# Performance work log

Hardware: AMD Instinct MI355X
Metric: run time of the kernel (lower is better)

## Reference

```python
import jax, jax.numpy as jnp
import numpy as np

N_NODES = 100000


def setup_inputs() -> dict:
    key = jax.random.key(0)
    ks = jax.random.split(key, 9)
    E = 1600000
    x = jax.random.normal(ks[0], (N_NODES, 12), dtype=jnp.float32)
    edge_index = jax.random.randint(ks[1], (2, E), 0, N_NODES, dtype=jnp.int64)
    def glorot(k, shape):
        lim = float(np.sqrt(6.0 / (shape[0] + shape[1])))
        return jax.random.uniform(k, shape, jnp.float32, -lim, lim)
    return {
        "x": x,
        "edge_index": edge_index,
        "W1": glorot(ks[2], (12, 64)),
        "b1": jnp.zeros((64,), jnp.float32),
        "W2": glorot(ks[3], (64, 128)),
        "b2": jnp.zeros((128,), jnp.float32),
        "W3": glorot(ks[4], (128, 96)),
        "b3": jnp.zeros((96,), jnp.float32),
    }


def reference(x, edge_index, W1, b1, W2, b2, W3, b3):
    N = x.shape[0]
    F_channel, n_his = 8, 12
    src, dst = edge_index[0], edge_index[1]
    # add self loops (PyG GCNConv default)
    loop = jnp.arange(N, dtype=src.dtype)
    src = jnp.concatenate([src, loop])
    dst = jnp.concatenate([dst, loop])
    # symmetric normalization: norm_e = deg[src]^-1/2 * deg[dst]^-1/2
    deg = jax.ops.segment_sum(jnp.ones_like(src, dtype=x.dtype), dst, num_segments=N)
    dinv = jnp.where(deg > 0, jax.lax.rsqrt(deg), 0.0)
    norm = dinv[src] * dinv[dst]  # [E+N]

    def gcn(h, W, b):
        hw = h @ W  # transform first (out_ch <= in-edge fanout cost)
        agg = jax.ops.segment_sum(hw[src] * norm[:, None], dst, num_segments=N)
        return agg + b

    h = jax.nn.relu(gcn(x, W1, b1))
    h = jax.nn.relu(gcn(h, W2, b2))
    h = gcn(h, W3, b3)
    return h.reshape(N, F_channel, n_his)
```

## Files before the change

### kernel.cpp

```cpp
#include <hip/hip_runtime.h>
#include <hip/hip_bf16.h>
#include <hip/hip_fp16.h>


static inline int cdiv(int a, int b) { return (a + b - 1) / b; }
constexpr int BLOCK = 256;
constexpr int BSHIFT = 9;
constexpr int BNODES = 1 << BSHIFT;

typedef float nfloat4 __attribute__((ext_vector_type(4)));
typedef _Float16 f16x8 __attribute__((ext_vector_type(8)));
typedef float f32x16 __attribute__((ext_vector_type(16)));


__global__ void zero_int_kernel(int* __restrict__ p, int n) {
    int i = blockIdx.x * blockDim.x + threadIdx.x;
    if (i < n) p[i] = 0;
}

__device__ __forceinline__ void nt_store_raw16(void* p, float4 v) {
    nfloat4 nv;
    nv.x = v.x; nv.y = v.y; nv.z = v.z; nv.w = v.w;
    __builtin_nontemporal_store(nv, (nfloat4*)p);
}

struct h4 { __half2 a, b; };
__device__ __forceinline__ void store_h4(__half* p, float4 v) {
    h4 r;
    r.a = __floats2half2_rn(v.x, v.y);
    r.b = __floats2half2_rn(v.z, v.w);
    *(h4*)p = r;
}

__device__ __forceinline__ void h8_add(float* acc, float4 raw) {
    union { float4 f; __half2 h[4]; } u;
    u.f = raw;
#pragma unroll
    for (int j = 0; j < 4; ++j) {
        float2 p = __half22float2(u.h[j]);
        acc[2 * j] += p.x;
        acc[2 * j + 1] += p.y;
    }
}


template <int CHUNK>
__global__ void bucket_count_kernel(const int* __restrict__ dst, int E,
                                    int* __restrict__ bcnt, int NB) {
    __shared__ int cnt[256];
    for (int i = threadIdx.x; i < NB; i += blockDim.x) cnt[i] = 0;
    __syncthreads();
    const int e0 = blockIdx.x * CHUNK;
    const int e1 = min(e0 + CHUNK, E);
    for (int e = e0 + threadIdx.x; e < e1; e += blockDim.x)
        atomicAdd(&cnt[dst[e] >> BSHIFT], 1);
    __syncthreads();
    for (int i = threadIdx.x; i < NB; i += blockDim.x)
        if (cnt[i]) atomicAdd(&bcnt[i], cnt[i]);
}

__global__ void bucket_scan_kernel(const int* __restrict__ bcnt, int* __restrict__ gbase,
                                   int* __restrict__ gcur, int NB) {
    __shared__ int tmp[256];
    int t = threadIdx.x;
    int v = (t < NB) ? bcnt[t] : 0;
    tmp[t] = v;
    __syncthreads();
    for (int off = 1; off < 256; off <<= 1) {
        int add = (t >= off) ? tmp[t - off] : 0;
        __syncthreads();
        tmp[t] += add;
        __syncthreads();
    }
    if (t < NB) { int ex = tmp[t] - v; gbase[t] = ex; gcur[t] = ex; }
}

template <int CHUNK>
__global__ void bin_edges_kernel(const int* __restrict__ ei, int E,
                                 int* __restrict__ gcur, unsigned* __restrict__ binned,
                                 int NB) {
    __shared__ int cnt[256], base[256], rk[256];
    for (int i = threadIdx.x; i < NB; i += blockDim.x) { cnt[i] = 0; rk[i] = 0; }
    __syncthreads();
    const int e0 = blockIdx.x * CHUNK;
    const int e1 = min(e0 + CHUNK, E);
    for (int e = e0 + threadIdx.x; e < e1; e += blockDim.x)
        atomicAdd(&cnt[ei[E + e] >> BSHIFT], 1);
    __syncthreads();
    for (int i = threadIdx.x; i < NB; i += blockDim.x)
        base[i] = atomicAdd(&gcur[i], cnt[i]);
    __syncthreads();
    for (int e = e0 + threadIdx.x; e < e1; e += blockDim.x) {
        int s = ei[e], d = ei[E + e];
        int b = d >> BSHIFT;
        int r = atomicAdd(&rk[b], 1);
        binned[base[b] + r] = (unsigned)s | ((unsigned)(d & (BNODES - 1)) << 17);
    }
}

__global__ void csr_fill_kernel(const int* __restrict__ gbase, const int* __restrict__ bcnt,
                                const unsigned* __restrict__ binned,
                                int* __restrict__ deg, float* __restrict__ dinv,
                                int* __restrict__ row_ptr, int* __restrict__ csr_src,
                                int* __restrict__ dh, int N) {
    __shared__ int c[BNODES];
    __shared__ int ps[256];
    __shared__ int dhloc[64];
    const int t = threadIdx.x;
    const int b = blockIdx.x;
    const int node0 = b << BSHIFT;
    c[t] = 0; c[t + 256] = 0;
    if (t < 64) dhloc[t] = 0;
    __syncthreads();
    const int base = gbase[b];
    const int end = base + bcnt[b];
    for (int e = base + t; e < end; e += 256)
        atomicAdd(&c[binned[e] >> 17], 1);
    __syncthreads();
    const int s0 = c[2 * t], s1 = c[2 * t + 1];
    const int pv = s0 + s1;
    ps[t] = pv;
    __syncthreads();
    for (int off = 1; off < 256; off <<= 1) {
        int add = (t >= off) ? ps[t - off] : 0;
        __syncthreads();
        ps[t] += add;
        __syncthreads();
    }
    const int ex = ps[t] - pv;
    const int p0 = base + ex;
    const int p1 = p0 + s0;
    const int n0 = node0 + 2 * t;
    if (n0 < N) {
        row_ptr[n0] = p0; deg[n0] = s0; dinv[n0] = rsqrtf((float)s0 + 1.0f);
        atomicAdd(&dhloc[min(s0, 63)], 1);
        if (n0 + 1 < N) {
            row_ptr[n0 + 1] = p1; deg[n0 + 1] = s1; dinv[n0 + 1] = rsqrtf((float)s1 + 1.0f);
            atomicAdd(&dhloc[min(s1, 63)], 1);
        }
    }
    c[2 * t] = p0; c[2 * t + 1] = p1;
    __syncthreads();
    if (t < 64 && dhloc[t]) atomicAdd(&dh[t], dhloc[t]);
    for (int e = base + t; e < end; e += 256) {
        unsigned sd = binned[e];
        int pos = atomicAdd(&c[sd >> 17], 1);
        csr_src[pos] = (int)(sd & 0x1FFFFu);
    }
}


__global__ void dscan_kernel(int* __restrict__ dh) {
    __shared__ int tmp[64];
    int t = threadIdx.x;
    int v = dh[t];
    tmp[t] = v;
    __syncthreads();
    for (int off = 1; off < 64; off <<= 1) {
        int add = (t >= off) ? tmp[t - off] : 0;
        __syncthreads();
        tmp[t] += add;
        __syncthreads();
    }
    dh[t] = tmp[t] - v;
}

__global__ void dperm_kernel(const int* __restrict__ deg, int* __restrict__ dh,
                             int* __restrict__ perm, int N) {
    __shared__ int cnt[64], base[64], rk[64];
    const int t = threadIdx.x;
    if (t < 64) { cnt[t] = 0; rk[t] = 0; }
    __syncthreads();
    const int i = blockIdx.x * blockDim.x + t;
    const int myb = (i < N) ? min(deg[i], 63) : -1;
    if (myb >= 0) atomicAdd(&cnt[myb], 1);
    __syncthreads();
    if (t < 64) base[t] = cnt[t] ? atomicAdd(&dh[t], cnt[t]) : 0;
    __syncthreads();
    if (myb >= 0) {
        int r = atomicAdd(&rk[myb], 1);
        perm[base[myb] + r] = i;
    }
}


__global__ void prescale_h_kernel(const float* __restrict__ x, const float* __restrict__ dinv,
                                  __half* __restrict__ xs, int N) {
    int i = blockIdx.x * blockDim.x + threadIdx.x;
    if (i >= N) return;
    float di = dinv[i];
    const float4* xr = (const float4*)(x + (size_t)i * 12);
    float4 a = xr[0], b = xr[1], c = xr[2];
    union { float4 f; __half2 h[4]; } u0, u1;
    u0.h[0] = __floats2half2_rn(a.x * di, a.y * di);
    u0.h[1] = __floats2half2_rn(a.z * di, a.w * di);
    u0.h[2] = __floats2half2_rn(b.x * di, b.y * di);
    u0.h[3] = __floats2half2_rn(b.z * di, b.w * di);
    u1.h[0] = __floats2half2_rn(c.x * di, c.y * di);
    u1.h[1] = __floats2half2_rn(c.z * di, c.w * di);
    u1.h[2] = __floats2half2_rn(0.f, 0.f);
    u1.h[3] = __floats2half2_rn(0.f, 0.f);
    float4* op = (float4*)(xs + (size_t)i * 16);
    op[0] = u0.f;
    op[1] = u1.f;
}


__device__ __forceinline__ void fma4(float4& acc, float s, const float4& w) {
    acc.x = fmaf(s, w.x, acc.x);
    acc.y = fmaf(s, w.y, acc.y);
    acc.z = fmaf(s, w.z, acc.z);
    acc.w = fmaf(s, w.w, acc.w);
}

__device__ __forceinline__ float4 epilogue4(float4 r, const float* bias, int c0,
                                            bool has_bias, bool relu, bool scale, float di) {
    if (has_bias) {
        const float4 bb = *(const float4*)(bias + c0);
        r.x += bb.x; r.y += bb.y; r.z += bb.z; r.w += bb.w;
    }
    if (relu) {
        r.x = fmaxf(r.x, 0.f); r.y = fmaxf(r.y, 0.f);
        r.z = fmaxf(r.z, 0.f); r.w = fmaxf(r.w, 0.f);
    }
    if (scale) { r.x *= di; r.y *= di; r.z *= di; r.w *= di; }
    return r;
}

template <int IN, int OUT, bool HAS_BIAS, bool RELU, bool SCALE, bool OUT_HALF>
__global__ void transform_kernel(const float* __restrict__ h, const float* __restrict__ W,
                                 const float* __restrict__ bias, const float* __restrict__ dinv,
                                 void* __restrict__ out_v, int N) {
    constexpr int CG = OUT / 4;
    constexpr int THREADS = 8 * CG;
    __shared__ float Ws[IN * OUT];
    for (int i = threadIdx.x; i < IN * OUT / 4; i += THREADS)
        ((float4*)Ws)[i] = ((const float4*)W)[i];
    __syncthreads();

    const int c0 = (threadIdx.x % CG) * 4;
    const int r0 = blockIdx.x * 32 + (threadIdx.x / CG) * 4;
    if (r0 >= N) return;

    const float* __restrict__ hr = h + (size_t)r0 * IN;
    float4 acc[4];
#pragma unroll
    for (int i = 0; i < 4; ++i) acc[i] = make_float4(0.f, 0.f, 0.f, 0.f);

#pragma unroll
    for (int k = 0; k < IN; k += 4) {
        float4 a[4];
#pragma unroll
        for (int i = 0; i < 4; ++i) a[i] = *(const float4*)(hr + (size_t)i * IN + k);
        const float4 w0 = *(const float4*)(Ws + (k + 0) * OUT + c0);
        const float4 w1 = *(const float4*)(Ws + (k + 1) * OUT + c0);
        const float4 w2 = *(const float4*)(Ws + (k + 2) * OUT + c0);
        const float4 w3 = *(const float4*)(Ws + (k + 3) * OUT + c0);
#pragma unroll
        for (int i = 0; i < 4; ++i) {
            fma4(acc[i], a[i].x, w0);
            fma4(acc[i], a[i].y, w1);
            fma4(acc[i], a[i].z, w2);
            fma4(acc[i], a[i].w, w3);
        }
    }

#pragma unroll
    for (int i = 0; i < 4; ++i) {
        float di = SCALE ? dinv[r0 + i] : 0.f;
        float4 r = epilogue4(acc[i], bias, c0, HAS_BIAS, RELU, SCALE, di);
        if (OUT_HALF)
            store_h4((__half*)out_v + (size_t)(r0 + i) * OUT + c0, r);
        else
            *(float4*)((float*)out_v + (size_t)(r0 + i) * OUT + c0) = r;
    }
}


__global__ void prep_w_kernel(const float* __restrict__ W2, const float* __restrict__ W3,
                              __half* __restrict__ W2T, __half* __restrict__ W3T) {
    int i = blockIdx.x * 256 + threadIdx.x;
    if (i < 64 * 128) {
        int k = i >> 7, n = i & 127;
        W2T[n * 64 + k] = __float2half(W2[i]);
    } else {
        int j = i - 64 * 128;
        if (j < 128 * 96) {
            int k = j / 96, n = j - k * 96;
            W3T[n * 128 + k] = __float2half(W3[j]);
        }
    }
}

__global__ void fused_t2t3_kernel(const __half* __restrict__ agg1,
                                  const __half* __restrict__ W2T,
                                  const float* __restrict__ b2,
                                  const __half* __restrict__ W3T,
                                  const float* __restrict__ dinv,
                                  __half* __restrict__ out,
                                  int N) {
    constexpr int LDH = 136;
    __shared__ _Float16 h2s[4][32 * LDH];
    const int lane = threadIdx.x & 63;
    const int wid = threadIdx.x >> 6;
    const int l31 = lane & 31;
    const int lh = lane >> 5;
    _Float16* hs = h2s[wid];

    float b2v[4];
#pragma unroll
    for (int nt = 0; nt < 4; ++nt) b2v[nt] = b2[nt * 32 + l31];

    const int NT = N >> 5;
    for (int t = blockIdx.x * 4 + wid; t < NT; t += gridDim.x * 4) {
        const int r0 = t << 5;

        f16x8 a2[4];
#pragma unroll
        for (int kb = 0; kb < 4; ++kb)
            a2[kb] = *(const f16x8*)(agg1 + (size_t)(r0 + l31) * 64 + kb * 16 + lh * 8);
#pragma unroll
        for (int nt = 0; nt < 4; ++nt) {
            f32x16 c = {0.f, 0.f, 0.f, 0.f, 0.f, 0.f, 0.f, 0.f,
                        0.f, 0.f, 0.f, 0.f, 0.f, 0.f, 0.f, 0.f};
#pragma unroll
            for (int kb = 0; kb < 4; ++kb) {
                f16x8 b = *(const f16x8*)(W2T + (size_t)(nt * 32 + l31) * 64 + kb * 16 + lh * 8);
                c = __builtin_amdgcn_mfma_f32_32x32x16_f16(a2[kb], b, c, 0, 0, 0);
            }
#pragma unroll
            for (int r = 0; r < 16; ++r) {
                int row = (r & 3) + 8 * (r >> 2) + 4 * lh;
                float v = fmaxf(c[r] + b2v[nt], 0.f);
                hs[row * LDH + nt * 32 + l31] = (_Float16)v;
            }
        }

        f16x8 a3[8];
#pragma unroll
        for (int kb = 0; kb < 8; ++kb)
            a3[kb] = *(const f16x8*)(hs + l31 * LDH + kb * 16 + lh * 8);
        float4 dv[4];
#pragma unroll
        for (int rg = 0; rg < 4; ++rg)
            dv[rg] = *(const float4*)(dinv + r0 + rg * 8 + lh * 4);
#pragma unroll
        for (int nt = 0; nt < 3; ++nt) {
            f32x16 c = {0.f, 0.f, 0.f, 0.f, 0.f, 0.f, 0.f, 0.f,
                        0.f, 0.f, 0.f, 0.f, 0.f, 0.f, 0.f, 0.f};
#pragma unroll
            for (int kb = 0; kb < 8; ++kb) {
                f16x8 b = *(const f16x8*)(W3T + (size_t)(nt * 32 + l31) * 128 + kb * 16 + lh * 8);
                c = __builtin_amdgcn_mfma_f32_32x32x16_f16(a3[kb], b, c, 0, 0, 0);
            }
#pragma unroll
            for (int r = 0; r < 16; ++r) {
                int row = (r & 3) + 8 * (r >> 2) + 4 * lh;
                float dvv = ((const float*)&dv[r >> 2])[r & 3];
                hs[row * LDH + nt * 32 + l31] = (_Float16)(c[r] * dvv);
            }
        }

#pragma unroll
        for (int it = 0; it < 6; ++it) {
            int id = lane + it * 64;
            int row = id / 12, ch = id - row * 12;
            float4 v = *(const float4*)(hs + row * LDH + ch * 8);
            *(float4*)((char*)(out + (size_t)r0 * 96) + (size_t)id * 16) = v;
        }
    }
}


__global__ void gather_x_kernel(const int* __restrict__ row_ptr, const int* __restrict__ deg,
                                const int* __restrict__ csr_src, const int* __restrict__ perm,
                                const float* __restrict__ dinv, const __half* __restrict__ xs,
                                float* __restrict__ out, int N) {
    int t = blockIdx.x * blockDim.x + threadIdx.x;
    if (t >= N * 2) return;
    int slot = t >> 1;
    int c = t & 1;
    int i = perm[N - 1 - slot];
    int f0 = c * 8;

    const int* __restrict__ sp = csr_src + row_ptr[i];
    int n = deg[i];
    float acc[8];
    {
        union { float4 f; __half2 h[4]; } u;
        u.f = *(const float4*)(xs + (size_t)i * 16 + f0);
#pragma unroll
        for (int j = 0; j < 4; ++j) {
            float2 p = __half22float2(u.h[j]);
            acc[2 * j] = p.x; acc[2 * j + 1] = p.y;
        }
    }

    int k = 0;
    if (n >= 8) {
        int s[8];
#pragma unroll
        for (int j = 0; j < 8; ++j) s[j] = sp[j];
        for (; k + 16 <= n; k += 8) {
            int ns[8];
#pragma unroll
            for (int j = 0; j < 8; ++j) ns[j] = sp[k + 8 + j];
            float4 v[8];
#pragma unroll
            for (int j = 0; j < 8; ++j) v[j] = *(const float4*)(xs + (size_t)s[j] * 16 + f0);
#pragma unroll
            for (int j = 0; j < 8; ++j) h8_add(acc, v[j]);
#pragma unroll
            for (int j = 0; j < 8; ++j) s[j] = ns[j];
        }
        float4 v[8];
#pragma unroll
        for (int j = 0; j < 8; ++j) v[j] = *(const float4*)(xs + (size_t)s[j] * 16 + f0);
#pragma unroll
        for (int j = 0; j < 8; ++j) h8_add(acc, v[j]);
        k += 8;
    }
    for (; k + 4 <= n; k += 4) {
        int s0 = sp[k + 0], s1 = sp[k + 1], s2 = sp[k + 2], s3 = sp[k + 3];
        float4 v0 = *(const float4*)(xs + (size_t)s0 * 16 + f0);
        float4 v1 = *(const float4*)(xs + (size_t)s1 * 16 + f0);
        float4 v2 = *(const float4*)(xs + (size_t)s2 * 16 + f0);
        float4 v3 = *(const float4*)(xs + (size_t)s3 * 16 + f0);
        h8_add(acc, v0); h8_add(acc, v1); h8_add(acc, v2); h8_add(acc, v3);
    }
    for (; k < n; ++k) {
        float4 v = *(const float4*)(xs + (size_t)sp[k] * 16 + f0);
        h8_add(acc, v);
    }

    float di = dinv[i];
    float* op = out + (size_t)i * 12;
    float4 r0;
    r0.x = acc[0] * di; r0.y = acc[1] * di; r0.z = acc[2] * di; r0.w = acc[3] * di;
    if (c == 0) {
        float4 r1;
        r1.x = acc[4] * di; r1.y = acc[5] * di; r1.z = acc[6] * di; r1.w = acc[7] * di;
        *(float4*)op = r0;
        *(float4*)(op + 4) = r1;
    } else {
        *(float4*)(op + 8) = r0;
    }
}

template <int F, bool HAS_BIAS, bool OUT_HALF>
__global__ void gather_h_kernel(const int* __restrict__ row_ptr, const int* __restrict__ deg,
                                const int* __restrict__ csr_src, const int* __restrict__ perm,
                                const float* __restrict__ dinv, const __half* __restrict__ hws,
                                const float* __restrict__ b, void* __restrict__ out_v, int N) {
    constexpr int TPN = F / 8;
    int t = blockIdx.x * blockDim.x + threadIdx.x;
    if (t >= N * TPN) return;
    int slot = t / TPN;
    int c = t - slot * TPN;
    int i = perm[N - 1 - slot];
    int f0 = c * 8;

    const int* __restrict__ sp = csr_src + row_ptr[i];
    int n = deg[i];
    float acc[8];
    {
        union { float4 f; __half2 h[4]; } u;
        u.f = *(const float4*)(hws + (size_t)i * F + f0);
#pragma unroll
        for (int j = 0; j < 4; ++j) {
            float2 p = __half22float2(u.h[j]);
            acc[2 * j] = p.x; acc[2 * j + 1] = p.y;
        }
    }

    int k = 0;
    if (n >= 8) {
        int s[8];
#pragma unroll
        for (int j = 0; j < 8; ++j) s[j] = sp[j];
        for (; k + 16 <= n; k += 8) {
            int ns[8];
#pragma unroll
            for (int j = 0; j < 8; ++j) ns[j] = sp[k + 8 + j];
            float4 v[8];
#pragma unroll
            for (int j = 0; j < 8; ++j) v[j] = *(const float4*)(hws + (size_t)s[j] * F + f0);
#pragma unroll
            for (int j = 0; j < 8; ++j) h8_add(acc, v[j]);
#pragma unroll
            for (int j = 0; j < 8; ++j) s[j] = ns[j];
        }
        float4 v[8];
#pragma unroll
        for (int j = 0; j < 8; ++j) v[j] = *(const float4*)(hws + (size_t)s[j] * F + f0);
#pragma unroll
        for (int j = 0; j < 8; ++j) h8_add(acc, v[j]);
        k += 8;
    }
    for (; k + 4 <= n; k += 4) {
        int s0 = sp[k + 0], s1 = sp[k + 1], s2 = sp[k + 2], s3 = sp[k + 3];
        float4 v0 = *(const float4*)(hws + (size_t)s0 * F + f0);
        float4 v1 = *(const float4*)(hws + (size_t)s1 * F + f0);
        float4 v2 = *(const float4*)(hws + (size_t)s2 * F + f0);
        float4 v3 = *(const float4*)(hws + (size_t)s3 * F + f0);
        h8_add(acc, v0); h8_add(acc, v1); h8_add(acc, v2); h8_add(acc, v3);
    }
    for (; k < n; ++k) {
        float4 v = *(const float4*)(hws + (size_t)sp[k] * F + f0);
        h8_add(acc, v);
    }

    float di = dinv[i];
    float4 r0, r1;
    if (HAS_BIAS) {
        const float4 bb0 = *(const float4*)(b + f0);
        const float4 bb1 = *(const float4*)(b + f0 + 4);
        r0.x = fmaf(acc[0], di, bb0.x); r0.y = fmaf(acc[1], di, bb0.y);
        r0.z = fmaf(acc[2], di, bb0.z); r0.w = fmaf(acc[3], di, bb0.w);
        r1.x = fmaf(acc[4], di, bb1.x); r1.y = fmaf(acc[5], di, bb1.y);
        r1.z = fmaf(acc[6], di, bb1.z); r1.w = fmaf(acc[7], di, bb1.w);
    } else {
        r0.x = acc[0] * di; r0.y = acc[1] * di; r0.z = acc[2] * di; r0.w = acc[3] * di;
        r1.x = acc[4] * di; r1.y = acc[5] * di; r1.z = acc[6] * di; r1.w = acc[7] * di;
    }
    if (OUT_HALF) {
        union { float4 f; __half2 h[4]; } u;
        u.h[0] = __floats2half2_rn(r0.x, r0.y);
        u.h[1] = __floats2half2_rn(r0.z, r0.w);
        u.h[2] = __floats2half2_rn(r1.x, r1.y);
        u.h[3] = __floats2half2_rn(r1.z, r1.w);
        nt_store_raw16((__half*)out_v + (size_t)i * F + f0, u.f);
    } else {
        float* op = (float*)out_v + (size_t)i * F + f0;
        nt_store_raw16(op, r0);
        nt_store_raw16(op + 4, r1);
    }
}


extern "C" void kernel_launch(void* const* d_in, const int* in_sizes, int n_in,
                              void* d_out, int out_size, void* d_ws, size_t ws_size,
                              hipStream_t stream) {
    const float* x  = (const float*)d_in[0];
    const int*   ei = (const int*)d_in[1];
    const float* W1 = (const float*)d_in[2];
    const float* b1 = (const float*)d_in[3];
    const float* W2 = (const float*)d_in[4];
    const float* b2 = (const float*)d_in[5];
    const float* W3 = (const float*)d_in[6];
    const float* b3 = (const float*)d_in[7];
    float* out = (float*)d_out;

    const int N = in_sizes[0] / 12;
    const int E = in_sizes[1] / 2;
    const int NB = cdiv(N, BNODES);

    char* ws = (char*)d_ws;
    int*   deg     = (int*)ws;    ws += (size_t)N * sizeof(int);
    int*   row_ptr = (int*)ws;    ws += (size_t)N * sizeof(int);
    int*   perm    = (int*)ws;    ws += (size_t)N * sizeof(int);
    int*   bcnt    = (int*)ws;    ws += 256 * sizeof(int);
    int*   dh      = (int*)ws;    ws += 64 * sizeof(int);
    int*   gbase   = (int*)ws;    ws += 256 * sizeof(int);
    int*   gcur    = (int*)ws;    ws += 256 * sizeof(int);
    float* dinv    = (float*)ws;  ws += (size_t)N * sizeof(float);
    __half* W2Th   = (__half*)ws; ws += 128 * 64 * sizeof(__half);
    __half* W3Th   = (__half*)ws; ws += 96 * 128 * sizeof(__half);
    int*   csr_src = (int*)ws;    ws += (size_t)E * sizeof(int);
    float* bufA    = (float*)ws;  ws += (size_t)N * 128 * sizeof(float);
    float* bufB    = (float*)ws;
    unsigned* binned = (unsigned*)bufB;

    zero_int_kernel<<<2, 256, 0, stream>>>(bcnt, 256 + 64);
    prep_w_kernel<<<80, 256, 0, stream>>>(W2, W3, W2Th, W3Th);
    bucket_count_kernel<4096><<<cdiv(E, 4096), BLOCK, 0, stream>>>(ei + E, E, bcnt, NB);
    bucket_scan_kernel<<<1, 256, 0, stream>>>(bcnt, gbase, gcur, NB);
    bin_edges_kernel<4096><<<cdiv(E, 4096), BLOCK, 0, stream>>>(ei, E, gcur, binned, NB);
    csr_fill_kernel<<<NB, 256, 0, stream>>>(gbase, bcnt, binned, deg, dinv, row_ptr,
                                            csr_src, dh, N);

    dscan_kernel<<<1, 64, 0, stream>>>(dh);
    dperm_kernel<<<cdiv(N, BLOCK), BLOCK, 0, stream>>>(deg, dh, perm, N);

    const int tb = cdiv(N, 32);

    prescale_h_kernel<<<cdiv(N, BLOCK), BLOCK, 0, stream>>>(x, dinv, (__half*)bufA, N);
    gather_x_kernel<<<cdiv(N * 2, BLOCK), BLOCK, 0, stream>>>(
        row_ptr, deg, csr_src, perm, dinv, (const __half*)bufA, bufB, N);
    transform_kernel<12, 64, true, true, true, true><<<tb, 8 * (64 / 4), 0, stream>>>(
        bufB, W1, b1, dinv, bufA, N);

    gather_h_kernel<64, false, true><<<cdiv(N * 8, BLOCK), BLOCK, 0, stream>>>(
        row_ptr, deg, csr_src, perm, dinv, (const __half*)bufA, nullptr, bufB, N);

    fused_t2t3_kernel<<<cdiv(N / 32, 8), 256, 0, stream>>>(
        (const __half*)bufB, W2Th, b2, W3Th, dinv, (__half*)bufA, N);

    gather_h_kernel<96, true, false><<<cdiv(N * 12, BLOCK), BLOCK, 0, stream>>>(
        row_ptr, deg, csr_src, perm, dinv, (const __half*)bufA, b3, out, N);
}
```

Baseline: 330.5 us.

## Precompute packed per-slot node headers and widen CSR build blocks

Adds a kernel that builds, once per call, an int4 header per degree-sorted slot holding row_ptr, degree, node id and dinv. The three gather kernels then read one coalesced 16-byte load instead of a perm lookup followed by three dependent scattered loads. The CSR fill kernel also moves to 1024-thread blocks, and the bucket count and bin kernels process 8192 edges per block. The cost is an extra launch and N*16 bytes of workspace.

```diff
diff --git a/kernel.cpp b/kernel.cpp
--- a/kernel.cpp
+++ b/kernel.cpp
@@ -109,40 +109,44 @@
     const int t = threadIdx.x;
     const int b = blockIdx.x;
     const int node0 = b << BSHIFT;
-    c[t] = 0; c[t + 256] = 0;
+    if (t < BNODES) c[t] = 0;
     if (t < 64) dhloc[t] = 0;
     __syncthreads();
     const int base = gbase[b];
     const int end = base + bcnt[b];
-    for (int e = base + t; e < end; e += 256)
+    for (int e = base + t; e < end; e += 1024)
         atomicAdd(&c[binned[e] >> 17], 1);
     __syncthreads();
-    const int s0 = c[2 * t], s1 = c[2 * t + 1];
-    const int pv = s0 + s1;
-    ps[t] = pv;
+    int s0 = 0, s1 = 0;
+    if (t < 256) {
+        s0 = c[2 * t]; s1 = c[2 * t + 1];
+        ps[t] = s0 + s1;
+    }
     __syncthreads();
     for (int off = 1; off < 256; off <<= 1) {
-        int add = (t >= off) ? ps[t - off] : 0;
+        int add = (t >= off && t < 256) ? ps[t - off] : 0;
         __syncthreads();
-        ps[t] += add;
+        if (t < 256) ps[t] += add;
         __syncthreads();
     }
-    const int ex = ps[t] - pv;
-    const int p0 = base + ex;
-    const int p1 = p0 + s0;
-    const int n0 = node0 + 2 * t;
-    if (n0 < N) {
-        row_ptr[n0] = p0; deg[n0] = s0; dinv[n0] = rsqrtf((float)s0 + 1.0f);
-        atomicAdd(&dhloc[min(s0, 63)], 1);
-        if (n0 + 1 < N) {
-            row_ptr[n0 + 1] = p1; deg[n0 + 1] = s1; dinv[n0 + 1] = rsqrtf((float)s1 + 1.0f);
-            atomicAdd(&dhloc[min(s1, 63)], 1);
-        }
-    }
-    c[2 * t] = p0; c[2 * t + 1] = p1;
+    if (t < 256) {
+        const int ex = ps[t] - (s0 + s1);
+        const int p0 = base + ex;
+        const int p1 = p0 + s0;
+        const int n0 = node0 + 2 * t;
+        if (n0 < N) {
+            row_ptr[n0] = p0; deg[n0] = s0; dinv[n0] = rsqrtf((float)s0 + 1.0f);
+            atomicAdd(&dhloc[min(s0, 63)], 1);
+            if (n0 + 1 < N) {
+                row_ptr[n0 + 1] = p1; deg[n0 + 1] = s1; dinv[n0 + 1] = rsqrtf((float)s1 + 1.0f);
+                atomicAdd(&dhloc[min(s1, 63)], 1);
+            }
+        }
+        c[2 * t] = p0; c[2 * t + 1] = p1;
+    }
     __syncthreads();
     if (t < 64 && dhloc[t]) atomicAdd(&dh[t], dhloc[t]);
-    for (int e = base + t; e < end; e += 256) {
+    for (int e = base + t; e < end; e += 1024) {
         unsigned sd = binned[e];
         int pos = atomicAdd(&c[sd >> 17], 1);
         csr_src[pos] = (int)(sd & 0x1FFFFu);
@@ -181,6 +185,20 @@
         int r = atomicAdd(&rk[myb], 1);
         perm[base[myb] + r] = i;
     }
+}
+
+__global__ void hdr_kernel(const int* __restrict__ perm, const int* __restrict__ row_ptr,
+                           const int* __restrict__ deg, const float* __restrict__ dinv,
+                           int4* __restrict__ hdr, int N) {
+    int slot = blockIdx.x * blockDim.x + threadIdx.x;
+    if (slot >= N) return;
+    int i = perm[N - 1 - slot];
+    int4 h;
+    h.x = row_ptr[i];
+    h.y = deg[i];
+    h.z = i;
+    h.w = __float_as_int(dinv[i]);
+    hdr[slot] = h;
 }
 
 
@@ -372,19 +390,20 @@
 }
 
 
-__global__ void gather_x_kernel(const int* __restrict__ row_ptr, const int* __restrict__ deg,
-                                const int* __restrict__ csr_src, const int* __restrict__ perm,
-                                const float* __restrict__ dinv, const __half* __restrict__ xs,
+__global__ void gather_x_kernel(const int4* __restrict__ hdr, const int* __restrict__ csr_src,
+                                const __half* __restrict__ xs,
                                 float* __restrict__ out, int N) {
     int t = blockIdx.x * blockDim.x + threadIdx.x;
     if (t >= N * 2) return;
     int slot = t >> 1;
     int c = t & 1;
-    int i = perm[N - 1 - slot];
+    const int4 H = hdr[slot];
+    const int* __restrict__ sp = csr_src + H.x;
+    const int n = H.y;
+    const int i = H.z;
+    const float di = __int_as_float(H.w);
     int f0 = c * 8;
 
-    const int* __restrict__ sp = csr_src + row_ptr[i];
-    int n = deg[i];
     float acc[8];
     {
         union { float4 f; __half2 h[4]; } u;
@@ -433,7 +452,6 @@
         h8_add(acc, v);
     }
 
-    float di = dinv[i];
     float* op = out + (size_t)i * 12;
     float4 r0;
     r0.x = acc[0] * di; r0.y = acc[1] * di; r0.z = acc[2] * di; r0.w = acc[3] * di;
@@ -448,20 +466,21 @@
 }
 
 template <int F, bool HAS_BIAS, bool OUT_HALF>
-__global__ void gather_h_kernel(const int* __restrict__ row_ptr, const int* __restrict__ deg,
-                                const int* __restrict__ csr_src, const int* __restrict__ perm,
-                                const float* __restrict__ dinv, const __half* __restrict__ hws,
+__global__ void gather_h_kernel(const int4* __restrict__ hdr, const int* __restrict__ csr_src,
+                                const __half* __restrict__ hws,
                                 const float* __restrict__ b, void* __restrict__ out_v, int N) {
     constexpr int TPN = F / 8;
     int t = blockIdx.x * blockDim.x + threadIdx.x;
     if (t >= N * TPN) return;
     int slot = t / TPN;
     int c = t - slot * TPN;
-    int i = perm[N - 1 - slot];
+    const int4 H = hdr[slot];
+    const int* __restrict__ sp = csr_src + H.x;
+    const int n = H.y;
+    const int i = H.z;
+    const float di = __int_as_float(H.w);
     int f0 = c * 8;
 
-    const int* __restrict__ sp = csr_src + row_ptr[i];
-    int n = deg[i];
     float acc[8];
     {
         union { float4 f; __half2 h[4]; } u;
@@ -510,7 +529,6 @@
         h8_add(acc, v);
     }
 
-    float di = dinv[i];
     float4 r0, r1;
     if (HAS_BIAS) {
         const float4 bb0 = *(const float4*)(b + f0);
@@ -564,6 +582,7 @@
     int*   gbase   = (int*)ws;    ws += 256 * sizeof(int);
     int*   gcur    = (int*)ws;    ws += 256 * sizeof(int);
     float* dinv    = (float*)ws;  ws += (size_t)N * sizeof(float);
+    int4*  hdr     = (int4*)ws;   ws += (size_t)N * sizeof(int4);
     __half* W2Th   = (__half*)ws; ws += 128 * 64 * sizeof(__half);
     __half* W3Th   = (__half*)ws; ws += 96 * 128 * sizeof(__half);
     int*   csr_src = (int*)ws;    ws += (size_t)E * sizeof(int);
@@ -573,29 +592,30 @@
 
     zero_int_kernel<<<2, 256, 0, stream>>>(bcnt, 256 + 64);
     prep_w_kernel<<<80, 256, 0, stream>>>(W2, W3, W2Th, W3Th);
-    bucket_count_kernel<4096><<<cdiv(E, 4096), BLOCK, 0, stream>>>(ei + E, E, bcnt, NB);
+    bucket_count_kernel<8192><<<cdiv(E, 8192), BLOCK, 0, stream>>>(ei + E, E, bcnt, NB);
     bucket_scan_kernel<<<1, 256, 0, stream>>>(bcnt, gbase, gcur, NB);
-    bin_edges_kernel<4096><<<cdiv(E, 4096), BLOCK, 0, stream>>>(ei, E, gcur, binned, NB);
-    csr_fill_kernel<<<NB, 256, 0, stream>>>(gbase, bcnt, binned, deg, dinv, row_ptr,
-                                            csr_src, dh, N);
+    bin_edges_kernel<8192><<<cdiv(E, 8192), BLOCK, 0, stream>>>(ei, E, gcur, binned, NB);
+    csr_fill_kernel<<<NB, 1024, 0, stream>>>(gbase, bcnt, binned, deg, dinv, row_ptr,
+                                             csr_src, dh, N);
 
     dscan_kernel<<<1, 64, 0, stream>>>(dh);
     dperm_kernel<<<cdiv(N, BLOCK), BLOCK, 0, stream>>>(deg, dh, perm, N);
+    hdr_kernel<<<cdiv(N, BLOCK), BLOCK, 0, stream>>>(perm, row_ptr, deg, dinv, hdr, N);
 
     const int tb = cdiv(N, 32);
 
     prescale_h_kernel<<<cdiv(N, BLOCK), BLOCK, 0, stream>>>(x, dinv, (__half*)bufA, N);
     gather_x_kernel<<<cdiv(N * 2, BLOCK), BLOCK, 0, stream>>>(
-        row_ptr, deg, csr_src, perm, dinv, (const __half*)bufA, bufB, N);
+        hdr, csr_src, (const __half*)bufA, bufB, N);
     transform_kernel<12, 64, true, true, true, true><<<tb, 8 * (64 / 4), 0, stream>>>(
         bufB, W1, b1, dinv, bufA, N);
 
     gather_h_kernel<64, false, true><<<cdiv(N * 8, BLOCK), BLOCK, 0, stream>>>(
-        row_ptr, deg, csr_src, perm, dinv, (const __half*)bufA, nullptr, bufB, N);
+        hdr, csr_src, (const __half*)bufA, nullptr, bufB, N);
 
     fused_t2t3_kernel<<<cdiv(N / 32, 8), 256, 0, stream>>>(
         (const __half*)bufB, W2Th, b2, W3Th, dinv, (__half*)bufA, N);
 
     gather_h_kernel<96, true, false><<<cdiv(N * 12, BLOCK), BLOCK, 0, stream>>>(
-        row_ptr, deg, csr_src, perm, dinv, (const __half*)bufA, b3, out, N);
-}
+        hdr, csr_src, (const __half*)bufA, b3, out, N);
+}
```

Measured after the change: 324.0 us. 2.0% less time.
